# Optimization experiments

Hardware: AMD Instinct MI355X
Metric: run time of the kernel (lower is better)

## Reference

```python
import jax, jax.numpy as jnp
import numpy as np

D_MODEL = 768
NUM_HEADS = 12
D_K = D_MODEL // NUM_HEADS


def setup_inputs() -> dict:
    key = jax.random.key(0)
    ks = jax.random.split(key, 11)
    B, S = 2, 2048
    scale = 1.0 / np.sqrt(D_MODEL)
    inp = {
        'query': jax.random.normal(ks[0], (B, S, D_MODEL), jnp.float32),
        'key': jax.random.normal(ks[1], (B, S, D_MODEL), jnp.float32),
        'value': jax.random.normal(ks[2], (B, S, D_MODEL), jnp.float32),
        # Linear params (torch nn.Linear: y = x @ W.T + b); store as [in,out]
        'Wq': jax.random.normal(ks[3], (D_MODEL, D_MODEL), jnp.float32) * scale,
        'bq': jnp.zeros((D_MODEL,), jnp.float32),
        'Wk': jax.random.normal(ks[4], (D_MODEL, D_MODEL), jnp.float32) * scale,
        'bk': jnp.zeros((D_MODEL,), jnp.float32),
        'Wv': jax.random.normal(ks[5], (D_MODEL, D_MODEL), jnp.float32) * scale,
        'bv': jnp.zeros((D_MODEL,), jnp.float32),
        'Wo': jax.random.normal(ks[6], (D_MODEL, D_MODEL), jnp.float32) * scale,
        'bo': jnp.zeros((D_MODEL,), jnp.float32),
    }
    return inp


def _split_heads(x):
    B, S, _ = x.shape
    return x.reshape(B, S, NUM_HEADS, D_K).transpose(0, 2, 1, 3)  # [B,H,S,d_k]


def reference(query, key, value, Wq, bq, Wk, bk, Wv, bv, Wo, bo):
    q = _split_heads(query @ Wq + bq)
    k = _split_heads(key @ Wk + bk)
    v = _split_heads(value @ Wv + bv)
    scores = jnp.einsum('bhqd,bhkd->bhqk', q, k) / np.sqrt(D_K)  # [B,H,S,S]
    attn = jax.nn.softmax(scores, axis=-1)
    x = jnp.einsum('bhqk,bhkd->bhqd', attn, v)  # [B,H,S,d_k]
    B, H, S, _ = x.shape
    x = x.transpose(0, 2, 1, 3).reshape(B, S, D_MODEL)
    return x @ Wo + bo
```

## Files before the change

### kernel.cpp

```cpp
#include <hip/hip_runtime.h>
#include <hip/hip_bf16.h>

#define DM     768
#define HEADS  12
#define DK     64
#define SQ     2048
#define BATCH  2
#define ROWS   4096
#define KTILES 24

typedef __attribute__((ext_vector_type(4))) float f32x4;
typedef __bf16 bf16x8 __attribute__((ext_vector_type(8)));
typedef unsigned short u16x8 __attribute__((ext_vector_type(8)));

#define QSCALE 0.180336880f

static __device__ __forceinline__ unsigned short f2bf(float f) {
    union { float f; unsigned u; } v; v.f = f;
    unsigned u = v.u;
    unsigned lsb = (u >> 16) & 1u;
    u += 0x7fffu + lsb;
    return (unsigned short)(u >> 16);
}

static __device__ __forceinline__ unsigned pack_bf16(float a, float b) {
    __hip_bfloat162 h = __float22bfloat162_rn(make_float2(a, b));
    unsigned u;
    __builtin_memcpy(&u, &h, 4);
    return u;
}

static __device__ __forceinline__ float fexp2(float x) {
#if __has_builtin(__builtin_amdgcn_exp2f)
    return __builtin_amdgcn_exp2f(x);
#else
    return exp2f(x);
#endif
}

static __device__ __forceinline__ bf16x8 load_bf16x8(const unsigned short* p) {
    u16x8 u = *(const u16x8*)p;
    return __builtin_bit_cast(bf16x8, u);
}

static __device__ __forceinline__ void gld_lds16(const unsigned short* g, unsigned short* l) {
    __builtin_amdgcn_global_load_lds((const __attribute__((address_space(1))) void*)g,
                                     (__attribute__((address_space(3))) void*)l,
                                     16, 0, 0);
}

static __device__ __forceinline__ void drain_dma() {
    asm volatile("s_waitcnt vmcnt(0)" ::: "memory");
}

__global__ __launch_bounds__(256) void cvt_frag3(const float* __restrict__ X0,
                                                 const float* __restrict__ X1,
                                                 const float* __restrict__ X2,
                                                 unsigned short* __restrict__ A0,
                                                 unsigned short* __restrict__ A1,
                                                 unsigned short* __restrict__ A2) {
    int z = blockIdx.z;
    const float* X = z == 0 ? X0 : z == 1 ? X1 : X2;
    unsigned short* A = z == 0 ? A0 : z == 1 ? A1 : A2;
    int p = blockIdx.x * 256 + threadIdx.x;
    int lane = p & 63;
    int g = p >> 6;
    int ks = g % KTILES;
    int mt = g / KTILES;
    int row = mt * 16 + (lane & 15);
    int k   = ks * 32 + (lane >> 4) * 8;
    const float* src = X + (size_t)row * DM + k;
    float4 v0 = *(const float4*)src;
    float4 v1 = *(const float4*)(src + 4);
    u16x8 o;
    o[0]=f2bf(v0.x); o[1]=f2bf(v0.y); o[2]=f2bf(v0.z); o[3]=f2bf(v0.w);
    o[4]=f2bf(v1.x); o[5]=f2bf(v1.y); o[6]=f2bf(v1.z); o[7]=f2bf(v1.w);
    *(u16x8*)(A + (size_t)p * 8) = o;
}

__global__ __launch_bounds__(256) void wt_frag4(const float* __restrict__ W0,
                                                const float* __restrict__ W1,
                                                const float* __restrict__ W2,
                                                const float* __restrict__ W3,
                                                unsigned short* __restrict__ F0,
                                                unsigned short* __restrict__ F1,
                                                unsigned short* __restrict__ F2,
                                                unsigned short* __restrict__ F3) {
    int z = blockIdx.z;
    const float* W = z == 0 ? W0 : z == 1 ? W1 : z == 2 ? W2 : W3;
    unsigned short* F = z == 0 ? F0 : z == 1 ? F1 : z == 2 ? F2 : F3;
    int p = blockIdx.x * 256 + threadIdx.x;
    int lane = p & 63;
    int t = (p >> 6) & 3;
    int g = p >> 8;
    int ks = g % KTILES;
    int nb = g / KTILES;
    int n = nb * 64 + t * 16 + (lane & 15);
    int k = ks * 32 + (lane >> 4) * 8;
    u16x8 o;
#pragma unroll
    for (int j = 0; j < 8; ++j) o[j] = f2bf(W[(size_t)(k + j) * DM + n]);
    *(u16x8*)(F + (size_t)p * 8) = o;
}

__global__ __launch_bounds__(256) void gemm_qkv(const unsigned short* __restrict__ A0,
                                                const unsigned short* __restrict__ A1,
                                                const unsigned short* __restrict__ A2,
                                                const unsigned short* __restrict__ F0,
                                                const unsigned short* __restrict__ F1,
                                                const unsigned short* __restrict__ F2,
                                                const float* __restrict__ b0,
                                                const float* __restrict__ b1,
                                                const float* __restrict__ b2,
                                                unsigned short* __restrict__ Qo,
                                                unsigned short* __restrict__ Ko,
                                                unsigned short* __restrict__ Vo) {
    __shared__ __align__(16) unsigned short ldsB[2][8192];

    int z = blockIdx.z;
    const unsigned short* A = z == 0 ? A0 : z == 1 ? A1 : A2;
    const unsigned short* F = z == 0 ? F0 : z == 1 ? F1 : F2;
    const float* bias        = z == 0 ? b0 : z == 1 ? b1 : b2;

    int w    = threadIdx.x >> 6;
    int lane = threadIdx.x & 63;
    int l15  = lane & 15;
    int quad = lane >> 4;
    int m0 = blockIdx.y * 128 + w * 32;
    int nb = blockIdx.x;
    int mt0 = m0 >> 4;

    const unsigned short* Ap = A + (size_t)mt0 * KTILES * 512 + lane * 8;
    const unsigned short* Bsrc = F + (size_t)nb * KTILES * 4 * 512 + w * 2048 + lane * 8;
    unsigned short* Bdst = &ldsB[0][w * 2048];

    f32x4 acc[2][4];
#pragma unroll
    for (int i = 0; i < 2; ++i)
#pragma unroll
        for (int t = 0; t < 4; ++t) acc[i][t] = (f32x4){0.f, 0.f, 0.f, 0.f};

#define BSTAGE(buf, c) do { \
        _Pragma("unroll") \
        for (int j = 0; j < 4; ++j) \
            gld_lds16(Bsrc + (size_t)(c) * 8192 + j * 512, Bdst + (buf) * 8192 + j * 512); \
    } while (0)

    BSTAGE(0, 0);

    bf16x8 a_cur[2][4];
#pragma unroll
    for (int k4 = 0; k4 < 4; ++k4)
#pragma unroll
        for (int i = 0; i < 2; ++i)
            a_cur[i][k4] = load_bf16x8(Ap + ((size_t)i * KTILES + k4) * 512);

    for (int c = 0; c < 6; ++c) {
        drain_dma();
        __syncthreads();
        if (c < 5) BSTAGE((c + 1) & 1, c + 1);
        const unsigned short* Bl = &ldsB[c & 1][0];
#pragma unroll
        for (int k4 = 0; k4 < 4; ++k4) {
#pragma unroll
            for (int t = 0; t < 4; ++t) {
                bf16x8 bb = load_bf16x8(Bl + (k4 * 4 + t) * 512 + lane * 8);
#pragma unroll
                for (int i = 0; i < 2; ++i)
                    acc[i][t] = __builtin_amdgcn_mfma_f32_16x16x32_bf16(a_cur[i][k4], bb, acc[i][t], 0, 0, 0);
            }
            if (c < 5) {
#pragma unroll
                for (int i = 0; i < 2; ++i)
                    a_cur[i][k4] = load_bf16x8(Ap + ((size_t)i * KTILES + (c + 1) * 4 + k4) * 512);
            }
        }
    }
#undef BSTAGE

    float scale = (z == 0) ? QSCALE : 1.0f;
#pragma unroll
    for (int t = 0; t < 4; ++t) {
        int col = nb * 64 + t * 16 + l15;
        float bv = bias[col];
        int h = col >> 6, d = col & (DK - 1);
#pragma unroll
        for (int i = 0; i < 2; ++i)
#pragma unroll
            for (int r = 0; r < 4; ++r) {
                int row = m0 + i * 16 + quad * 4 + r;
                float v = (acc[i][t][r] + bv) * scale;
                int bb = row >> 11, s = row & (SQ - 1);
                size_t bh = (size_t)(bb * HEADS + h);
                if (z == 0) {
                    Qo[(bh * SQ + s) * DK + d] = f2bf(v);
                } else if (z == 1) {
                    int sc = s & 63;
                    Ko[(bh * (SQ / 64) + (s >> 6)) * 4096 + sc * 64 +
                       (((d >> 3) ^ ((sc >> 1) & 7)) << 3) + (d & 7)] = f2bf(v);
                } else {
                    int sc = s & 63;
                    Vo[(bh * (SQ / 64) + (s >> 6)) * 4096 + d * 64 +
                       (((sc >> 3) ^ ((d >> 1) & 7)) << 3) + (sc & 7)] = f2bf(v);
                }
            }
    }
}

__global__ __launch_bounds__(256) void flash_attn(const unsigned short* __restrict__ Q,
                                                  const unsigned short* __restrict__ Kb,
                                                  const unsigned short* __restrict__ Vb,
                                                  unsigned short* __restrict__ Af) {
    __shared__ __align__(16) unsigned short ldsP[4][32 * 72];
    __shared__ __align__(16) float fO[2][2048];
    __shared__ __align__(16) float fL[2][512];

    int w    = threadIdx.x >> 6;
    int lane = threadIdx.x & 63;
    int l15  = lane & 15;
    int quad = lane >> 4;
    int rg   = w >> 1;
    int par  = w & 1;

    int lin  = blockIdx.x;
    int nlin = (lin & 7) * 96 + (lin >> 3);
    int q0   = (nlin & 31) * 64 + rg * 32;
    int h    = (nlin >> 5) % HEADS;
    int b    = nlin / (32 * HEADS);

    size_t bh = (size_t)(b * HEADS + h);
    const unsigned short* Qp = Q  + (bh * SQ + q0) * DK;
    const unsigned short* KB = Kb + bh * (SQ / 64) * 4096;
    const unsigned short* VB = Vb + bh * (SQ / 64) * 4096;

    bf16x8 aq[2][2];
#pragma unroll
    for (int i = 0; i < 2; ++i) {
        aq[i][0] = load_bf16x8(Qp + (i * 16 + l15) * DK + quad * 8);
        aq[i][1] = load_bf16x8(Qp + (i * 16 + l15) * DK + 32 + quad * 8);
    }

    f32x4 o[2][4];
#pragma unroll
    for (int i = 0; i < 2; ++i)
#pragma unroll
        for (int t = 0; t < 4; ++t) o[i][t] = (f32x4){0.f, 0.f, 0.f, 0.f};
    float lsum[2][4] = {{0.f,0.f,0.f,0.f},{0.f,0.f,0.f,0.f}};

    unsigned short* Pw = &ldsP[w][0];

    int koff[4][2], voff[4][2];
#pragma unroll
    for (int t = 0; t < 4; ++t) {
        int pr = (t >> 1) * 32 + 2 * l15 + (t & 1);
        int sw = l15 & 7;
        koff[t][0] = pr * 64 + (((quad)     ^ sw) << 3);
        koff[t][1] = pr * 64 + (((4 + quad) ^ sw) << 3);
        int d = t * 16 + l15;
        int swv = (l15 >> 1) & 7;
        voff[t][0] = d * 64 + (((quad)     ^ swv) << 3);
        voff[t][1] = d * 64 + (((4 + quad) ^ swv) << 3);
    }

    u16x8 kreg[8], vreg[8];
#define LOADK(n) do { \
        const unsigned short* kc_ = KB + (size_t)(n) * 4096; \
        _Pragma("unroll") \
        for (int t = 0; t < 4; ++t) { \
            kreg[2 * t]     = *(const u16x8*)(kc_ + koff[t][0]); \
            kreg[2 * t + 1] = *(const u16x8*)(kc_ + koff[t][1]); \
        } \
    } while (0)
#define LOADV(n) do { \
        const unsigned short* vc_ = VB + (size_t)(n) * 4096; \
        _Pragma("unroll") \
        for (int t = 0; t < 4; ++t) { \
            vreg[2 * t]     = *(const u16x8*)(vc_ + voff[t][0]); \
            vreg[2 * t + 1] = *(const u16x8*)(vc_ + voff[t][1]); \
        } \
    } while (0)

    LOADK(par);
    LOADV(par);

    for (int s = 0; s < 16; ++s) {
        f32x4 sc[2][4];
#pragma unroll
        for (int i = 0; i < 2; ++i)
#pragma unroll
            for (int t = 0; t < 4; ++t) sc[i][t] = (f32x4){0.f, 0.f, 0.f, 0.f};

        __builtin_amdgcn_s_setprio(1);
#pragma unroll
        for (int t = 0; t < 4; ++t) {
            bf16x8 k0 = __builtin_bit_cast(bf16x8, kreg[2 * t]);
            bf16x8 k1 = __builtin_bit_cast(bf16x8, kreg[2 * t + 1]);
#pragma unroll
            for (int i = 0; i < 2; ++i) {
                sc[i][t] = __builtin_amdgcn_mfma_f32_16x16x32_bf16(aq[i][0], k0, sc[i][t], 0, 0, 0);
                sc[i][t] = __builtin_amdgcn_mfma_f32_16x16x32_bf16(aq[i][1], k1, sc[i][t], 0, 0, 0);
            }
        }
        __builtin_amdgcn_s_setprio(0);

        if (s < 15) LOADK(2 * s + 2 + par);

#pragma unroll
        for (int i = 0; i < 2; ++i)
#pragma unroll
            for (int sub = 0; sub < 2; ++sub)
#pragma unroll
                for (int r = 0; r < 4; ++r) {
                    float e0 = fexp2(sc[i][2 * sub][r]);
                    float e1 = fexp2(sc[i][2 * sub + 1][r]);
                    lsum[i][r] += e0 + e1;
                    *(unsigned*)(Pw + (i * 16 + quad * 4 + r) * 72 + sub * 32 + l15 * 2)
                        = pack_bf16(e0, e1);
                }

        bf16x8 pf[2][2];
#pragma unroll
        for (int i = 0; i < 2; ++i) {
            pf[i][0] = load_bf16x8(Pw + (i * 16 + l15) * 72 + quad * 8);
            pf[i][1] = load_bf16x8(Pw + (i * 16 + l15) * 72 + 32 + quad * 8);
        }

        __builtin_amdgcn_s_setprio(1);
#pragma unroll
        for (int t = 0; t < 4; ++t) {
            bf16x8 v0 = __builtin_bit_cast(bf16x8, vreg[2 * t]);
            bf16x8 v1 = __builtin_bit_cast(bf16x8, vreg[2 * t + 1]);
#pragma unroll
            for (int i = 0; i < 2; ++i) {
                o[i][t] = __builtin_amdgcn_mfma_f32_16x16x32_bf16(pf[i][0], v0, o[i][t], 0, 0, 0);
                o[i][t] = __builtin_amdgcn_mfma_f32_16x16x32_bf16(pf[i][1], v1, o[i][t], 0, 0, 0);
            }
        }
        __builtin_amdgcn_s_setprio(0);

        if (s < 15) LOADV(2 * s + 2 + par);
    }
#undef LOADK
#undef LOADV

    if (par == 1) {
#pragma unroll
        for (int i = 0; i < 2; ++i)
#pragma unroll
            for (int r = 0; r < 4; ++r) {
                int rowin = i * 16 + quad * 4 + r;
#pragma unroll
                for (int t = 0; t < 4; ++t)
                    fO[rg][rowin * 64 + t * 16 + l15] = o[i][t][r];
                fL[rg][rowin * 16 + l15] = lsum[i][r];
            }
    }
    __syncthreads();
    if (par == 0) {
#pragma unroll
        for (int i = 0; i < 2; ++i)
#pragma unroll
            for (int r = 0; r < 4; ++r) {
                int rowin = i * 16 + quad * 4 + r;
                float l = lsum[i][r] + fL[rg][rowin * 16 + l15];
                l += __shfl_xor(l, 1);
                l += __shfl_xor(l, 2);
                l += __shfl_xor(l, 4);
                l += __shfl_xor(l, 8);
                float inv = 1.0f / l;
                int R  = b * SQ + q0 + rowin;
                int mt = R >> 4;
#pragma unroll
                for (int t = 0; t < 4; ++t) {
                    float val = o[i][t][r] + fO[rg][rowin * 64 + t * 16 + l15];
                    int ks    = h * 2 + (t >> 1);
                    int quadp = ((t & 1) << 1) + (l15 >> 3);
                    int j     = l15 & 7;
                    Af[(size_t)(mt * KTILES + ks) * 512 +
                       (size_t)((quadp << 4) + (rowin & 15)) * 8 + j] = f2bf(val * inv);
                }
            }
    }
}

__global__ __launch_bounds__(256) void gemm_out(const unsigned short* __restrict__ Af,
                                                const unsigned short* __restrict__ Ff,
                                                const float* __restrict__ bias,
                                                float* __restrict__ out) {
    __shared__ __align__(16) unsigned short ldsB[2][8192];

    int w    = threadIdx.x >> 6;
    int lane = threadIdx.x & 63;
    int l15  = lane & 15;
    int quad = lane >> 4;
    int m0 = blockIdx.y * 64 + w * 16;
    int nb = blockIdx.x;
    int mt = m0 >> 4;

    const unsigned short* Ap = Af + (size_t)mt * KTILES * 512 + lane * 8;
    const unsigned short* Bsrc = Ff + (size_t)nb * KTILES * 4 * 512 + w * 2048 + lane * 8;
    unsigned short* Bdst = &ldsB[0][w * 2048];

    f32x4 acc[4];
#pragma unroll
    for (int t = 0; t < 4; ++t) acc[t] = (f32x4){0.f, 0.f, 0.f, 0.f};

#define BSTAGE(buf, c) do { \
        _Pragma("unroll") \
        for (int j = 0; j < 4; ++j) \
            gld_lds16(Bsrc + (size_t)(c) * 8192 + j * 512, Bdst + (buf) * 8192 + j * 512); \
    } while (0)

    BSTAGE(0, 0);

    bf16x8 a_cur[4];
#pragma unroll
    for (int k4 = 0; k4 < 4; ++k4)
        a_cur[k4] = load_bf16x8(Ap + (size_t)k4 * 512);

    for (int c = 0; c < 6; ++c) {
        drain_dma();
        __syncthreads();
        if (c < 5) BSTAGE((c + 1) & 1, c + 1);
        const unsigned short* Bl = &ldsB[c & 1][0];
#pragma unroll
        for (int k4 = 0; k4 < 4; ++k4) {
#pragma unroll
            for (int t = 0; t < 4; ++t) {
                bf16x8 bb = load_bf16x8(Bl + (k4 * 4 + t) * 512 + lane * 8);
                acc[t] = __builtin_amdgcn_mfma_f32_16x16x32_bf16(a_cur[k4], bb, acc[t], 0, 0, 0);
            }
            if (c < 5)
                a_cur[k4] = load_bf16x8(Ap + (size_t)((c + 1) * 4 + k4) * 512);
        }
    }
#undef BSTAGE

#pragma unroll
    for (int t = 0; t < 4; ++t) {
        int col = nb * 64 + t * 16 + l15;
        float bv = bias[col];
#pragma unroll
        for (int r = 0; r < 4; ++r) {
            int row = m0 + quad * 4 + r;
            out[(size_t)row * DM + col] = acc[t][r] + bv;
        }
    }
}

extern "C" void kernel_launch(void* const* d_in, const int* in_sizes, int n_in,
                              void* d_out, int out_size, void* d_ws, size_t ws_size,
                              hipStream_t stream) {
    const float* query = (const float*)d_in[0];
    const float* key   = (const float*)d_in[1];
    const float* value = (const float*)d_in[2];
    const float* Wq = (const float*)d_in[3];  const float* bq = (const float*)d_in[4];
    const float* Wk = (const float*)d_in[5];  const float* bk = (const float*)d_in[6];
    const float* Wv = (const float*)d_in[7];  const float* bv = (const float*)d_in[8];
    const float* Wo = (const float*)d_in[9];  const float* bo = (const float*)d_in[10];

    const size_t NX = (size_t)ROWS * DM;
    const size_t NW = (size_t)DM * DM;
    unsigned short* Xq  = (unsigned short*)d_ws;
    unsigned short* Xk  = Xq  + NX;
    unsigned short* Xv  = Xk  + NX;
    unsigned short* Qb  = Xv  + NX;
    unsigned short* Kb  = Qb  + NX;
    unsigned short* Vt  = Kb  + NX;
    unsigned short* Wtq = Vt  + NX;
    unsigned short* Wtk = Wtq + NW;
    unsigned short* Wtv = Wtk + NW;
    unsigned short* Wto = Wtv + NW;

    cvt_frag3<<<dim3((unsigned)(NX / 8 / 256), 1, 3), 256, 0, stream>>>(
        query, key, value, Xq, Xk, Xv);

    wt_frag4<<<dim3((unsigned)(NW / 8 / 256), 1, 4), 256, 0, stream>>>(
        Wq, Wk, Wv, Wo, Wtq, Wtk, Wtv, Wto);

    gemm_qkv<<<dim3(DM / 64, ROWS / 128, 3), 256, 0, stream>>>(
        Xq, Xk, Xv, Wtq, Wtk, Wtv, bq, bk, bv, Qb, Kb, Vt);

    flash_attn<<<dim3((SQ / 64) * HEADS * BATCH, 1, 1), 256, 0, stream>>>(Qb, Kb, Vt, Xq);

    gemm_out<<<dim3(DM / 64, ROWS / 64), 256, 0, stream>>>(Xq, Wto, bo, (float*)d_out);
}
```

Before: 201.8 us.

## Merge prep kernels and restructure V loads in flash attention for occupancy

Merges the two conversion kernels (activation and weight bf16 fragmenting) into one launch with a flat block index, removing one kernel launch. In flash attention, V tile loads move from a one-step-ahead prefetch into two half loads issued inside the current iteration, and the per-step offset arrays shrink by deriving the second half offset with XOR. launch_bounds(256,4) is added to cap registers. The aim is lower register pressure and higher occupancy, at the cost of exposing V load latency within each iteration.

Result: slower. 302.1 us (+49.7%).

```diff
diff --git a/kernel.cpp b/kernel.cpp
--- a/kernel.cpp
+++ b/kernel.cpp
@@ -53,54 +53,59 @@
     asm volatile("s_waitcnt vmcnt(0)" ::: "memory");
 }
 
-__global__ __launch_bounds__(256) void cvt_frag3(const float* __restrict__ X0,
-                                                 const float* __restrict__ X1,
-                                                 const float* __restrict__ X2,
-                                                 unsigned short* __restrict__ A0,
-                                                 unsigned short* __restrict__ A1,
-                                                 unsigned short* __restrict__ A2) {
-    int z = blockIdx.z;
-    const float* X = z == 0 ? X0 : z == 1 ? X1 : X2;
-    unsigned short* A = z == 0 ? A0 : z == 1 ? A1 : A2;
-    int p = blockIdx.x * 256 + threadIdx.x;
-    int lane = p & 63;
-    int g = p >> 6;
-    int ks = g % KTILES;
-    int mt = g / KTILES;
-    int row = mt * 16 + (lane & 15);
-    int k   = ks * 32 + (lane >> 4) * 8;
-    const float* src = X + (size_t)row * DM + k;
-    float4 v0 = *(const float4*)src;
-    float4 v1 = *(const float4*)(src + 4);
-    u16x8 o;
-    o[0]=f2bf(v0.x); o[1]=f2bf(v0.y); o[2]=f2bf(v0.z); o[3]=f2bf(v0.w);
-    o[4]=f2bf(v1.x); o[5]=f2bf(v1.y); o[6]=f2bf(v1.z); o[7]=f2bf(v1.w);
-    *(u16x8*)(A + (size_t)p * 8) = o;
-}
-
-__global__ __launch_bounds__(256) void wt_frag4(const float* __restrict__ W0,
-                                                const float* __restrict__ W1,
-                                                const float* __restrict__ W2,
-                                                const float* __restrict__ W3,
-                                                unsigned short* __restrict__ F0,
-                                                unsigned short* __restrict__ F1,
-                                                unsigned short* __restrict__ F2,
-                                                unsigned short* __restrict__ F3) {
-    int z = blockIdx.z;
-    const float* W = z == 0 ? W0 : z == 1 ? W1 : z == 2 ? W2 : W3;
-    unsigned short* F = z == 0 ? F0 : z == 1 ? F1 : z == 2 ? F2 : F3;
-    int p = blockIdx.x * 256 + threadIdx.x;
-    int lane = p & 63;
-    int t = (p >> 6) & 3;
-    int g = p >> 8;
-    int ks = g % KTILES;
-    int nb = g / KTILES;
-    int n = nb * 64 + t * 16 + (lane & 15);
-    int k = ks * 32 + (lane >> 4) * 8;
-    u16x8 o;
-#pragma unroll
-    for (int j = 0; j < 8; ++j) o[j] = f2bf(W[(size_t)(k + j) * DM + n]);
-    *(u16x8*)(F + (size_t)p * 8) = o;
+__global__ __launch_bounds__(256) void prep(const float* __restrict__ X0,
+                                            const float* __restrict__ X1,
+                                            const float* __restrict__ X2,
+                                            const float* __restrict__ W0,
+                                            const float* __restrict__ W1,
+                                            const float* __restrict__ W2,
+                                            const float* __restrict__ W3,
+                                            unsigned short* __restrict__ A0,
+                                            unsigned short* __restrict__ A1,
+                                            unsigned short* __restrict__ A2,
+                                            unsigned short* __restrict__ F0,
+                                            unsigned short* __restrict__ F1,
+                                            unsigned short* __restrict__ F2,
+                                            unsigned short* __restrict__ F3) {
+    int blk = blockIdx.x;
+    if (blk < 4608) {
+        int z  = blk / 1536;
+        int pb = blk - z * 1536;
+        const float* X = z == 0 ? X0 : z == 1 ? X1 : X2;
+        unsigned short* A = z == 0 ? A0 : z == 1 ? A1 : A2;
+        int p = pb * 256 + threadIdx.x;
+        int lane = p & 63;
+        int g = p >> 6;
+        int ks = g % KTILES;
+        int mt = g / KTILES;
+        int row = mt * 16 + (lane & 15);
+        int k   = ks * 32 + (lane >> 4) * 8;
+        const float* src = X + (size_t)row * DM + k;
+        float4 v0 = *(const float4*)src;
+        float4 v1 = *(const float4*)(src + 4);
+        u16x8 o;
+        o[0]=f2bf(v0.x); o[1]=f2bf(v0.y); o[2]=f2bf(v0.z); o[3]=f2bf(v0.w);
+        o[4]=f2bf(v1.x); o[5]=f2bf(v1.y); o[6]=f2bf(v1.z); o[7]=f2bf(v1.w);
+        *(u16x8*)(A + (size_t)p * 8) = o;
+    } else {
+        int q  = blk - 4608;
+        int z  = q / 288;
+        int pb = q - z * 288;
+        const float* W = z == 0 ? W0 : z == 1 ? W1 : z == 2 ? W2 : W3;
+        unsigned short* F = z == 0 ? F0 : z == 1 ? F1 : z == 2 ? F2 : F3;
+        int p = pb * 256 + threadIdx.x;
+        int lane = p & 63;
+        int t = (p >> 6) & 3;
+        int g = p >> 8;
+        int ks = g % KTILES;
+        int nb = g / KTILES;
+        int n = nb * 64 + t * 16 + (lane & 15);
+        int k = ks * 32 + (lane >> 4) * 8;
+        u16x8 o;
+#pragma unroll
+        for (int j = 0; j < 8; ++j) o[j] = f2bf(W[(size_t)(k + j) * DM + n]);
+        *(u16x8*)(F + (size_t)p * 8) = o;
+    }
 }
 
 __global__ __launch_bounds__(256) void gemm_qkv(const unsigned short* __restrict__ A0,
@@ -207,10 +212,10 @@
     }
 }
 
-__global__ __launch_bounds__(256) void flash_attn(const unsigned short* __restrict__ Q,
-                                                  const unsigned short* __restrict__ Kb,
-                                                  const unsigned short* __restrict__ Vb,
-                                                  unsigned short* __restrict__ Af) {
+__global__ __launch_bounds__(256, 4) void flash_attn(const unsigned short* __restrict__ Q,
+                                                     const unsigned short* __restrict__ Kb,
+                                                     const unsigned short* __restrict__ Vb,
+                                                     unsigned short* __restrict__ Af) {
     __shared__ __align__(16) unsigned short ldsP[4][32 * 72];
     __shared__ __align__(16) float fO[2][2048];
     __shared__ __align__(16) float fL[2][512];
@@ -249,41 +254,29 @@
 
     unsigned short* Pw = &ldsP[w][0];
 
-    int koff[4][2], voff[4][2];
+    int kof[4], vof[4];
 #pragma unroll
     for (int t = 0; t < 4; ++t) {
         int pr = (t >> 1) * 32 + 2 * l15 + (t & 1);
-        int sw = l15 & 7;
-        koff[t][0] = pr * 64 + (((quad)     ^ sw) << 3);
-        koff[t][1] = pr * 64 + (((4 + quad) ^ sw) << 3);
+        kof[t] = pr * 64 + (((quad) ^ (l15 & 7)) << 3);
         int d = t * 16 + l15;
-        int swv = (l15 >> 1) & 7;
-        voff[t][0] = d * 64 + (((quad)     ^ swv) << 3);
-        voff[t][1] = d * 64 + (((4 + quad) ^ swv) << 3);
-    }
-
-    u16x8 kreg[8], vreg[8];
+        vof[t] = d * 64 + (((quad) ^ ((l15 >> 1) & 7)) << 3);
+    }
+
+    u16x8 kreg[8], vh1[4], vh2[4];
 #define LOADK(n) do { \
         const unsigned short* kc_ = KB + (size_t)(n) * 4096; \
         _Pragma("unroll") \
         for (int t = 0; t < 4; ++t) { \
-            kreg[2 * t]     = *(const u16x8*)(kc_ + koff[t][0]); \
-            kreg[2 * t + 1] = *(const u16x8*)(kc_ + koff[t][1]); \
+            kreg[2 * t]     = *(const u16x8*)(kc_ + kof[t]); \
+            kreg[2 * t + 1] = *(const u16x8*)(kc_ + (kof[t] ^ 32)); \
         } \
     } while (0)
-#define LOADV(n) do { \
-        const unsigned short* vc_ = VB + (size_t)(n) * 4096; \
-        _Pragma("unroll") \
-        for (int t = 0; t < 4; ++t) { \
-            vreg[2 * t]     = *(const u16x8*)(vc_ + voff[t][0]); \
-            vreg[2 * t + 1] = *(const u16x8*)(vc_ + voff[t][1]); \
-        } \
-    } while (0)
 
     LOADK(par);
-    LOADV(par);
 
     for (int s = 0; s < 16; ++s) {
+        int c = 2 * s + par;
         f32x4 sc[2][4];
 #pragma unroll
         for (int i = 0; i < 2; ++i)
@@ -303,7 +296,14 @@
         }
         __builtin_amdgcn_s_setprio(0);
 
-        if (s < 15) LOADK(2 * s + 2 + par);
+        if (s < 15) LOADK(c + 2);
+        {
+            const unsigned short* vc_ = VB + (size_t)c * 4096;
+            vh1[0] = *(const u16x8*)(vc_ + vof[0]);
+            vh1[1] = *(const u16x8*)(vc_ + (vof[0] ^ 32));
+            vh1[2] = *(const u16x8*)(vc_ + vof[1]);
+            vh1[3] = *(const u16x8*)(vc_ + (vof[1] ^ 32));
+        }
 
 #pragma unroll
         for (int i = 0; i < 2; ++i)
@@ -318,30 +318,31 @@
                         = pack_bf16(e0, e1);
                 }
 
-        bf16x8 pf[2][2];
+        {
+            const unsigned short* vc_ = VB + (size_t)c * 4096;
+            vh2[0] = *(const u16x8*)(vc_ + vof[2]);
+            vh2[1] = *(const u16x8*)(vc_ + (vof[2] ^ 32));
+            vh2[2] = *(const u16x8*)(vc_ + vof[3]);
+            vh2[3] = *(const u16x8*)(vc_ + (vof[3] ^ 32));
+        }
+
 #pragma unroll
         for (int i = 0; i < 2; ++i) {
-            pf[i][0] = load_bf16x8(Pw + (i * 16 + l15) * 72 + quad * 8);
-            pf[i][1] = load_bf16x8(Pw + (i * 16 + l15) * 72 + 32 + quad * 8);
-        }
-
-        __builtin_amdgcn_s_setprio(1);
-#pragma unroll
-        for (int t = 0; t < 4; ++t) {
-            bf16x8 v0 = __builtin_bit_cast(bf16x8, vreg[2 * t]);
-            bf16x8 v1 = __builtin_bit_cast(bf16x8, vreg[2 * t + 1]);
-#pragma unroll
-            for (int i = 0; i < 2; ++i) {
-                o[i][t] = __builtin_amdgcn_mfma_f32_16x16x32_bf16(pf[i][0], v0, o[i][t], 0, 0, 0);
-                o[i][t] = __builtin_amdgcn_mfma_f32_16x16x32_bf16(pf[i][1], v1, o[i][t], 0, 0, 0);
-            }
-        }
-        __builtin_amdgcn_s_setprio(0);
-
-        if (s < 15) LOADV(2 * s + 2 + par);
+            bf16x8 pf0 = load_bf16x8(Pw + (i * 16 + l15) * 72 + quad * 8);
+            bf16x8 pf1 = load_bf16x8(Pw + (i * 16 + l15) * 72 + 32 + quad * 8);
+            __builtin_amdgcn_s_setprio(1);
+            o[i][0] = __builtin_amdgcn_mfma_f32_16x16x32_bf16(pf0, __builtin_bit_cast(bf16x8, vh1[0]), o[i][0], 0, 0, 0);
+            o[i][0] = __builtin_amdgcn_mfma_f32_16x16x32_bf16(pf1, __builtin_bit_cast(bf16x8, vh1[1]), o[i][0], 0, 0, 0);
+            o[i][1] = __builtin_amdgcn_mfma_f32_16x16x32_bf16(pf0, __builtin_bit_cast(bf16x8, vh1[2]), o[i][1], 0, 0, 0);
+            o[i][1] = __builtin_amdgcn_mfma_f32_16x16x32_bf16(pf1, __builtin_bit_cast(bf16x8, vh1[3]), o[i][1], 0, 0, 0);
+            o[i][2] = __builtin_amdgcn_mfma_f32_16x16x32_bf16(pf0, __builtin_bit_cast(bf16x8, vh2[0]), o[i][2], 0, 0, 0);
+            o[i][2] = __builtin_amdgcn_mfma_f32_16x16x32_bf16(pf1, __builtin_bit_cast(bf16x8, vh2[1]), o[i][2], 0, 0, 0);
+            o[i][3] = __builtin_amdgcn_mfma_f32_16x16x32_bf16(pf0, __builtin_bit_cast(bf16x8, vh2[2]), o[i][3], 0, 0, 0);
+            o[i][3] = __builtin_amdgcn_mfma_f32_16x16x32_bf16(pf1, __builtin_bit_cast(bf16x8, vh2[3]), o[i][3], 0, 0, 0);
+            __builtin_amdgcn_s_setprio(0);
+        }
     }
 #undef LOADK
-#undef LOADV
 
     if (par == 1) {
 #pragma unroll
@@ -472,11 +473,9 @@
     unsigned short* Wtv = Wtk + NW;
     unsigned short* Wto = Wtv + NW;
 
-    cvt_frag3<<<dim3((unsigned)(NX / 8 / 256), 1, 3), 256, 0, stream>>>(
-        query, key, value, Xq, Xk, Xv);
-
-    wt_frag4<<<dim3((unsigned)(NW / 8 / 256), 1, 4), 256, 0, stream>>>(
-        Wq, Wk, Wv, Wo, Wtq, Wtk, Wtv, Wto);
+    prep<<<dim3(5760, 1, 1), 256, 0, stream>>>(
+        query, key, value, Wq, Wk, Wv, Wo,
+        Xq, Xk, Xv, Wtq, Wtk, Wtv, Wto);
 
     gemm_qkv<<<dim3(DM / 64, ROWS / 128, 3), 256, 0, stream>>>(
         Xq, Xk, Xv, Wtq, Wtk, Wtv, bq, bk, bv, Qb, Kb, Vt);
```

## Fuse input and weight prep kernels; stage activations through LDS; widen gemm_out tiles

Applied to the files above, without the earlier changes.

Merges the activation and weight bf16-conversion kernels into one launch. The activation path now reads each 16-row tile with coalesced float4 loads into LDS, then writes the fragment layout from LDS instead of doing strided global reads. gemm_out now computes two 16-row M tiles per wave (128 rows per block), reusing each B fragment loaded from LDS across both. This removes one launch and halves the number of output blocks, at the cost of more registers per thread and fewer blocks in flight.

Result: no change. 201.1 us (-0.3%).

```diff
diff --git a/kernel.cpp b/kernel.cpp
--- a/kernel.cpp
+++ b/kernel.cpp
@@ -12,6 +12,7 @@
 typedef __attribute__((ext_vector_type(4))) float f32x4;
 typedef __bf16 bf16x8 __attribute__((ext_vector_type(8)));
 typedef unsigned short u16x8 __attribute__((ext_vector_type(8)));
+typedef unsigned short u16x4 __attribute__((ext_vector_type(4)));
 
 #define QSCALE 0.180336880f
 
@@ -53,54 +54,71 @@
     asm volatile("s_waitcnt vmcnt(0)" ::: "memory");
 }
 
-__global__ __launch_bounds__(256) void cvt_frag3(const float* __restrict__ X0,
-                                                 const float* __restrict__ X1,
-                                                 const float* __restrict__ X2,
-                                                 unsigned short* __restrict__ A0,
-                                                 unsigned short* __restrict__ A1,
-                                                 unsigned short* __restrict__ A2) {
-    int z = blockIdx.z;
-    const float* X = z == 0 ? X0 : z == 1 ? X1 : X2;
-    unsigned short* A = z == 0 ? A0 : z == 1 ? A1 : A2;
-    int p = blockIdx.x * 256 + threadIdx.x;
-    int lane = p & 63;
-    int g = p >> 6;
-    int ks = g % KTILES;
-    int mt = g / KTILES;
-    int row = mt * 16 + (lane & 15);
-    int k   = ks * 32 + (lane >> 4) * 8;
-    const float* src = X + (size_t)row * DM + k;
-    float4 v0 = *(const float4*)src;
-    float4 v1 = *(const float4*)(src + 4);
-    u16x8 o;
-    o[0]=f2bf(v0.x); o[1]=f2bf(v0.y); o[2]=f2bf(v0.z); o[3]=f2bf(v0.w);
-    o[4]=f2bf(v1.x); o[5]=f2bf(v1.y); o[6]=f2bf(v1.z); o[7]=f2bf(v1.w);
-    *(u16x8*)(A + (size_t)p * 8) = o;
-}
-
-__global__ __launch_bounds__(256) void wt_frag4(const float* __restrict__ W0,
-                                                const float* __restrict__ W1,
-                                                const float* __restrict__ W2,
-                                                const float* __restrict__ W3,
-                                                unsigned short* __restrict__ F0,
-                                                unsigned short* __restrict__ F1,
-                                                unsigned short* __restrict__ F2,
-                                                unsigned short* __restrict__ F3) {
-    int z = blockIdx.z;
-    const float* W = z == 0 ? W0 : z == 1 ? W1 : z == 2 ? W2 : W3;
-    unsigned short* F = z == 0 ? F0 : z == 1 ? F1 : z == 2 ? F2 : F3;
-    int p = blockIdx.x * 256 + threadIdx.x;
-    int lane = p & 63;
-    int t = (p >> 6) & 3;
-    int g = p >> 8;
-    int ks = g % KTILES;
-    int nb = g / KTILES;
-    int n = nb * 64 + t * 16 + (lane & 15);
-    int k = ks * 32 + (lane >> 4) * 8;
-    u16x8 o;
-#pragma unroll
-    for (int j = 0; j < 8; ++j) o[j] = f2bf(W[(size_t)(k + j) * DM + n]);
-    *(u16x8*)(F + (size_t)p * 8) = o;
+#define LROW 776
+__global__ __launch_bounds__(256) void prep(const float* __restrict__ X0,
+                                            const float* __restrict__ X1,
+                                            const float* __restrict__ X2,
+                                            const float* __restrict__ W0,
+                                            const float* __restrict__ W1,
+                                            const float* __restrict__ W2,
+                                            const float* __restrict__ W3,
+                                            unsigned short* __restrict__ A0,
+                                            unsigned short* __restrict__ A1,
+                                            unsigned short* __restrict__ A2,
+                                            unsigned short* __restrict__ F0,
+                                            unsigned short* __restrict__ F1,
+                                            unsigned short* __restrict__ F2,
+                                            unsigned short* __restrict__ F3) {
+    __shared__ __align__(16) unsigned short lds[16 * LROW];
+    int blk = blockIdx.x;
+    int tid = threadIdx.x;
+    if (blk < 768) {
+        int z  = blk >> 8;
+        int mt = blk & 255;
+        const float* X = z == 0 ? X0 : z == 1 ? X1 : X2;
+        unsigned short* A = z == 0 ? A0 : z == 1 ? A1 : A2;
+        const float* src = X + (size_t)mt * 16 * DM;
+#pragma unroll
+        for (int i = 0; i < 12; ++i) {
+            int fi = tid + i * 256;
+            int row = fi / 192;
+            int c4  = fi - row * 192;
+            float4 v = *(const float4*)(src + (size_t)fi * 4);
+            u16x4 o;
+            o[0] = f2bf(v.x); o[1] = f2bf(v.y); o[2] = f2bf(v.z); o[3] = f2bf(v.w);
+            *(u16x4*)(&lds[row * LROW + c4 * 4]) = o;
+        }
+        __syncthreads();
+        unsigned short* out = A + (size_t)mt * KTILES * 512;
+#pragma unroll
+        for (int c = 0; c < 6; ++c) {
+            int idx  = tid + c * 256;
+            int ks   = idx >> 6;
+            int lane = idx & 63;
+            int r15  = lane & 15;
+            int qd   = lane >> 4;
+            u16x8 v = *(const u16x8*)(&lds[r15 * LROW + ks * 32 + qd * 8]);
+            *(u16x8*)(out + (size_t)idx * 8) = v;
+        }
+    } else {
+        int q  = blk - 768;
+        int z  = q / 288;
+        int pb = q - z * 288;
+        const float* W = z == 0 ? W0 : z == 1 ? W1 : z == 2 ? W2 : W3;
+        unsigned short* F = z == 0 ? F0 : z == 1 ? F1 : z == 2 ? F2 : F3;
+        int p = pb * 256 + tid;
+        int lane = p & 63;
+        int t = (p >> 6) & 3;
+        int g = p >> 8;
+        int ks = g % KTILES;
+        int nb = g / KTILES;
+        int n = nb * 64 + t * 16 + (lane & 15);
+        int k = ks * 32 + (lane >> 4) * 8;
+        u16x8 o;
+#pragma unroll
+        for (int j = 0; j < 8; ++j) o[j] = f2bf(W[(size_t)(k + j) * DM + n]);
+        *(u16x8*)(F + (size_t)p * 8) = o;
+    }
 }
 
 __global__ __launch_bounds__(256) void gemm_qkv(const unsigned short* __restrict__ A0,
@@ -393,17 +411,19 @@
     int lane = threadIdx.x & 63;
     int l15  = lane & 15;
     int quad = lane >> 4;
-    int m0 = blockIdx.y * 64 + w * 16;
+    int m0 = blockIdx.y * 128 + w * 32;
     int nb = blockIdx.x;
-    int mt = m0 >> 4;
-
-    const unsigned short* Ap = Af + (size_t)mt * KTILES * 512 + lane * 8;
+    int mt0 = m0 >> 4;
+
+    const unsigned short* Ap = Af + (size_t)mt0 * KTILES * 512 + lane * 8;
     const unsigned short* Bsrc = Ff + (size_t)nb * KTILES * 4 * 512 + w * 2048 + lane * 8;
     unsigned short* Bdst = &ldsB[0][w * 2048];
 
-    f32x4 acc[4];
-#pragma unroll
-    for (int t = 0; t < 4; ++t) acc[t] = (f32x4){0.f, 0.f, 0.f, 0.f};
+    f32x4 acc[2][4];
+#pragma unroll
+    for (int i = 0; i < 2; ++i)
+#pragma unroll
+        for (int t = 0; t < 4; ++t) acc[i][t] = (f32x4){0.f, 0.f, 0.f, 0.f};
 
 #define BSTAGE(buf, c) do { \
         _Pragma("unroll") \
@@ -413,10 +433,12 @@
 
     BSTAGE(0, 0);
 
-    bf16x8 a_cur[4];
+    bf16x8 a_cur[2][4];
 #pragma unroll
     for (int k4 = 0; k4 < 4; ++k4)
-        a_cur[k4] = load_bf16x8(Ap + (size_t)k4 * 512);
+#pragma unroll
+        for (int i = 0; i < 2; ++i)
+            a_cur[i][k4] = load_bf16x8(Ap + ((size_t)i * KTILES + k4) * 512);
 
     for (int c = 0; c < 6; ++c) {
         drain_dma();
@@ -428,10 +450,15 @@
 #pragma unroll
             for (int t = 0; t < 4; ++t) {
                 bf16x8 bb = load_bf16x8(Bl + (k4 * 4 + t) * 512 + lane * 8);
-                acc[t] = __builtin_amdgcn_mfma_f32_16x16x32_bf16(a_cur[k4], bb, acc[t], 0, 0, 0);
-            }
-            if (c < 5)
-                a_cur[k4] = load_bf16x8(Ap + (size_t)((c + 1) * 4 + k4) * 512);
+#pragma unroll
+                for (int i = 0; i < 2; ++i)
+                    acc[i][t] = __builtin_amdgcn_mfma_f32_16x16x32_bf16(a_cur[i][k4], bb, acc[i][t], 0, 0, 0);
+            }
+            if (c < 5) {
+#pragma unroll
+                for (int i = 0; i < 2; ++i)
+                    a_cur[i][k4] = load_bf16x8(Ap + ((size_t)i * KTILES + (c + 1) * 4 + k4) * 512);
+            }
         }
     }
 #undef BSTAGE
@@ -441,10 +468,12 @@
         int col = nb * 64 + t * 16 + l15;
         float bv = bias[col];
 #pragma unroll
-        for (int r = 0; r < 4; ++r) {
-            int row = m0 + quad * 4 + r;
-            out[(size_t)row * DM + col] = acc[t][r] + bv;
-        }
+        for (int i = 0; i < 2; ++i)
+#pragma unroll
+            for (int r = 0; r < 4; ++r) {
+                int row = m0 + i * 16 + quad * 4 + r;
+                out[(size_t)row * DM + col] = acc[i][t][r] + bv;
+            }
     }
 }
 
@@ -472,16 +501,14 @@
     unsigned short* Wtv = Wtk + NW;
     unsigned short* Wto = Wtv + NW;
 
-    cvt_frag3<<<dim3((unsigned)(NX / 8 / 256), 1, 3), 256, 0, stream>>>(
-        query, key, value, Xq, Xk, Xv);
-
-    wt_frag4<<<dim3((unsigned)(NW / 8 / 256), 1, 4), 256, 0, stream>>>(
-        Wq, Wk, Wv, Wo, Wtq, Wtk, Wtv, Wto);
+    prep<<<dim3(1920, 1, 1), 256, 0, stream>>>(
+        query, key, value, Wq, Wk, Wv, Wo,
+        Xq, Xk, Xv, Wtq, Wtk, Wtv, Wto);
 
     gemm_qkv<<<dim3(DM / 64, ROWS / 128, 3), 256, 0, stream>>>(
         Xq, Xk, Xv, Wtq, Wtk, Wtv, bq, bk, bv, Qb, Kb, Vt);
 
     flash_attn<<<dim3((SQ / 64) * HEADS * BATCH, 1, 1), 256, 0, stream>>>(Qb, Kb, Vt, Xq);
 
-    gemm_out<<<dim3(DM / 64, ROWS / 64), 256, 0, stream>>>(Xq, Wto, bo, (float*)d_out);
-}
+    gemm_out<<<dim3(DM / 64, ROWS / 128), 256, 0, stream>>>(Xq, Wto, bo, (float*)d_out);
+}
```
